# Kernel tuning notes

Hardware: AMD Instinct MI355X
Metric: run time of the kernel (lower is better)

The kernel has to match this reference:

```python
import jax, jax.numpy as jnp
import numpy as np

C = 256
H = 8
D = C // H


def setup_inputs() -> dict:
    key = jax.random.key(0)
    ks = jax.random.split(key, 6)
    scale = 1.0 / np.sqrt(C)
    x = jax.random.normal(ks[0], (8, C, 2048), dtype=jnp.float32)
    Wq = jax.random.normal(ks[1], (C, C), dtype=jnp.float32) * scale
    Wk = jax.random.normal(ks[2], (C, C), dtype=jnp.float32) * scale
    Wv = jax.random.normal(ks[3], (C, C), dtype=jnp.float32) * scale
    Wo = jax.random.normal(ks[4], (C, C), dtype=jnp.float32) * scale
    bo = jax.random.normal(ks[5], (C,), dtype=jnp.float32) * 0.01
    return {"x": x, "Wq": Wq, "Wk": Wk, "Wv": Wv, "Wo": Wo, "bo": bo}


def reference(x, Wq, Wk, Wv, Wo, bo):
    # x: [N, C, L]; Conv1d(k=1) == per-position matmul with weight [out, in]
    q = jnp.einsum('oc,ncl->nol', Wq, x)
    k = jnp.einsum('oc,ncl->nol', Wk, x)
    v = jnp.einsum('oc,ncl->nol', Wv, x)
    N, _, L = x.shape
    # rearrange 'n (h d) l -> n l h d'
    q = q.reshape(N, H, D, L).transpose(0, 3, 1, 2)
    k = k.reshape(N, H, D, L).transpose(0, 3, 1, 2)
    v = v.reshape(N, H, D, L).transpose(0, 3, 1, 2)
    qk = jnp.einsum('nqhd,nkhd->nhqk', q, k)
    # NOTE: original scales by full embedding size (channels), not head_dim
    attn = jax.nn.softmax(qk * (C ** -0.5), axis=3)
    out = jnp.einsum('nhql,nlhd->nqhd', attn, v)
    # rearrange 'n l h d -> n (h d) l'
    out = out.transpose(0, 2, 3, 1).reshape(N, C, L)
    return jnp.einsum('oc,ncl->nol', Wo, out) + bo[None, :, None]
```

## Files before the change

### kernel.cpp

```cpp
#include <hip/hip_runtime.h>


typedef __bf16 bf8 __attribute__((ext_vector_type(8)));
typedef float f4 __attribute__((ext_vector_type(4)));
typedef float f32x4 __attribute__((ext_vector_type(4)));
typedef unsigned short u16;
typedef unsigned int u32;
typedef u16 u16x4 __attribute__((ext_vector_type(4)));
typedef u16 u16x8 __attribute__((ext_vector_type(8)));
typedef u32 u32x4 __attribute__((ext_vector_type(4)));

__device__ __forceinline__ u16 f2bf(float f) {
  __bf16 h = (__bf16)f;
  return __builtin_bit_cast(u16, h);
}
__device__ __forceinline__ float bf2f(u16 b) {
  union { u32 u; float f; } v; v.u = ((u32)b) << 16;
  return v.f;
}
__device__ __forceinline__ u32 pk2bf(float a, float b) {
  return ((u32)f2bf(b) << 16) | (u32)f2bf(a);
}
__device__ __forceinline__ float exp2_fast(float x) {
  return __builtin_amdgcn_exp2f(x);
}

#define MFMA(a, b, c) __builtin_amdgcn_mfma_f32_16x16x32_bf16((a), (b), (c), 0, 0, 0)

__global__ __launch_bounds__(256) void convert_weights(
    const float* __restrict__ Wq, const float* __restrict__ Wk,
    const float* __restrict__ Wv, const float* __restrict__ Wo,
    const float* __restrict__ bo,
    u16* __restrict__ Wqb, u16* __restrict__ Wkb, u16* __restrict__ Wvb,
    u16* __restrict__ Wob, u16* __restrict__ bob) {
  const int tid = threadIdx.x;
  const int seg = blockIdx.x >> 6;
  const int blk = blockIdx.x & 63;
  const float* s; u16* d;
  if (seg == 0)      { s = Wq; d = Wqb; }
  else if (seg == 1) { s = Wk; d = Wkb; }
  else if (seg == 2) { s = Wv; d = Wvb; }
  else               { s = Wo; d = Wob; }
  const int base = blk * 1024 + tid * 4;
  f32x4 v = *(const f32x4*)(s + base);
  u16x4 o;
#pragma unroll
  for (int i = 0; i < 4; ++i) o[i] = f2bf(v[i]);
  *(u16x4*)(d + base) = o;
  if (blockIdx.x == 0 && tid < 64) {
    const int bb = tid * 4;
    f32x4 bv = *(const f32x4*)(bo + bb);
    u16x4 ob;
#pragma unroll
    for (int i = 0; i < 4; ++i) ob[i] = f2bf(bv[i]);
    *(u16x4*)(bob + bb) = ob;
  }
}

__global__ __launch_bounds__(256) void qkv_proj(
    const float* __restrict__ x, const u16* __restrict__ Wq,
    const u16* __restrict__ Wk, const u16* __restrict__ Wv,
    u16* __restrict__ qbuf, u16* __restrict__ kbuf, u16* __restrict__ vbuf) {
  __shared__ __align__(16) u16 xt[2][64 * 40];
  const int n = blockIdx.z;
  const int o0 = blockIdx.y * 64;
  const int l0 = blockIdx.x * 64;
  const int tid = threadIdx.x;
  const int w = tid >> 6, lane = tid & 63, quad = lane >> 4, l16 = lane & 15;
  const int ow = o0 + w * 16;

  f4 acc[3][4];
#pragma unroll
  for (int p = 0; p < 3; ++p)
#pragma unroll
    for (int lt = 0; lt < 4; ++lt) acc[p][lt] = (f4){0.f, 0.f, 0.f, 0.f};

  const int cp = tid >> 4;
  const int lq = (tid & 15) * 4;

  auto stage = [&](int c0, int buf) {
    const float* xp = x + (n * 256 + c0 + 2 * cp) * 2048 + l0 + lq;
    f32x4 r0 = *(const f32x4*)xp;
    f32x4 r1 = *(const f32x4*)(xp + 2048);
#pragma unroll
    for (int i = 0; i < 4; ++i)
      *(u32*)&xt[buf][(lq + i) * 40 + 2 * cp] = pk2bf(r0[i], r1[i]);
  };

  stage(0, 0);
  for (int s = 0; s < 8; ++s) {
    __syncthreads();
    if (s < 7) stage((s + 1) * 32, (s + 1) & 1);
    const int c0 = s * 32;
    bf8 a0 = *(const bf8*)(Wq + (ow + l16) * 256 + c0 + quad * 8);
    bf8 a1 = *(const bf8*)(Wk + (ow + l16) * 256 + c0 + quad * 8);
    bf8 a2 = *(const bf8*)(Wv + (ow + l16) * 256 + c0 + quad * 8);
    const u16* xb = xt[s & 1];
#pragma unroll
    for (int lt = 0; lt < 4; ++lt) {
      bf8 b = *(const bf8*)&xb[(lt * 16 + l16) * 40 + quad * 8];
      acc[0][lt] = MFMA(a0, b, acc[0][lt]);
      acc[1][lt] = MFMA(a1, b, acc[1][lt]);
      acc[2][lt] = MFMA(a2, b, acc[2][lt]);
    }
  }
#pragma unroll
  for (int lt = 0; lt < 4; ++lt) {
    const int l = l0 + lt * 16 + l16;
#pragma unroll
    for (int r = 0; r < 4; ++r) {
      const int o = ow + quad * 4 + r;
      const int qk_idx = ((n * 8 + (o >> 5)) * 2048 + l) * 32 + (o & 31);
      qbuf[qk_idx] = f2bf(acc[0][lt][r]);
      kbuf[qk_idx] = f2bf(acc[1][lt][r]);
      vbuf[(n * 256 + o) * 2048 + l] = f2bf(acc[2][lt][r]);
    }
  }
}

__global__ __launch_bounds__(256) void attn(
    const u16* __restrict__ qbuf, const u16* __restrict__ kbuf,
    const u16* __restrict__ vbuf, u16* __restrict__ abuf) {
  __shared__ __align__(16) u16 Klds[64 * 40];
  __shared__ __align__(16) u32 Vlds[32 * 36];
  __shared__ __align__(16) u32 Pb[4][32 * 36];
  const int head = blockIdx.x;
  const int n = head >> 3, h = head & 7;
  const int tid = threadIdx.x;
  const int w = tid >> 6, lane = tid & 63, quad = lane >> 4, l16 = lane & 15;
  const int q0 = blockIdx.y * 128 + w * 32;

  const u16* kb = kbuf + (size_t)head * 2048 * 32;
  const u16* vb = vbuf + ((size_t)n * 256 + h * 32) * 2048;
  u32* pb32 = Pb[w];
  const u16* pbu = (const u16*)Pb[w];
  const u16* vld16 = (const u16*)Vlds;

  bf8 aq[2];
  aq[0] = *(const bf8*)(qbuf + ((size_t)head * 2048 + q0 + l16) * 32 + quad * 8);
  aq[1] = *(const bf8*)(qbuf + ((size_t)head * 2048 + q0 + 16 + l16) * 32 + quad * 8);

  f4 O[2][2];
  float lsum[2][4];
#pragma unroll
  for (int qt = 0; qt < 2; ++qt) {
    O[qt][0] = (f4){0.f, 0.f, 0.f, 0.f};
    O[qt][1] = (f4){0.f, 0.f, 0.f, 0.f};
#pragma unroll
    for (int r = 0; r < 4; ++r) lsum[qt][r] = 0.f;
  }

  const int krow = tid >> 2, kcol = (tid & 3) * 8;
  const int vd = tid >> 3, vg = (tid & 7) >> 2, vcb = (tid & 3) * 4;

  const float SC = 0.09019327066650391f;

  for (int kc = 0; kc < 2048; kc += 64) {
    __syncthreads();
    *(u16x8*)&Klds[krow * 40 + kcol] = *(const u16x8*)(kb + (kc + krow) * 32 + kcol);
    {
      const u16* vp = vb + vd * 2048 + kc + vg * 32 + vcb;
      u16x4 lo = *(const u16x4*)vp;
      u16x4 hi = *(const u16x4*)(vp + 16);
      u32x4 pk;
#pragma unroll
      for (int i = 0; i < 4; ++i) pk[i] = ((u32)hi[i] << 16) | (u32)lo[i];
      *(u32x4*)&Vlds[vd * 36 + vg * 16 + vcb] = pk;
    }
    __syncthreads();

    bf8 bk[4];
#pragma unroll
    for (int b = 0; b < 4; ++b)
      bk[b] = *(const bf8*)&Klds[(b * 16 + l16) * 40 + quad * 8];

#pragma unroll
    for (int qt = 0; qt < 2; ++qt) {
      f4 z = (f4){0.f, 0.f, 0.f, 0.f};
      f4 s0 = MFMA(aq[qt], bk[0], z);
      f4 s1 = MFMA(aq[qt], bk[1], z);
      f4 s2 = MFMA(aq[qt], bk[2], z);
      f4 s3 = MFMA(aq[qt], bk[3], z);
      const int rowb = (qt * 16 + quad * 4) * 36 + l16;
#pragma unroll
      for (int r = 0; r < 4; ++r) {
        float e00 = exp2_fast(s0[r] * SC);
        float e01 = exp2_fast(s1[r] * SC);
        float e10 = exp2_fast(s2[r] * SC);
        float e11 = exp2_fast(s3[r] * SC);
        lsum[qt][r] += (e00 + e01) + (e10 + e11);
        pb32[rowb + r * 36]      = pk2bf(e00, e01);
        pb32[rowb + r * 36 + 16] = pk2bf(e10, e11);
      }
    }
    asm volatile("s_waitcnt lgkmcnt(0)" ::: "memory");
#pragma unroll
    for (int g = 0; g < 2; ++g) {
      bf8 bv0 = *(const bf8*)&vld16[l16 * 72 + g * 32 + quad * 8];
      bf8 bv1 = *(const bf8*)&vld16[(16 + l16) * 72 + g * 32 + quad * 8];
      bf8 ap0 = *(const bf8*)&pbu[l16 * 72 + g * 32 + quad * 8];
      bf8 ap1 = *(const bf8*)&pbu[(16 + l16) * 72 + g * 32 + quad * 8];
      O[0][0] = MFMA(ap0, bv0, O[0][0]);
      O[0][1] = MFMA(ap0, bv1, O[0][1]);
      O[1][0] = MFMA(ap1, bv0, O[1][0]);
      O[1][1] = MFMA(ap1, bv1, O[1][1]);
    }
  }

#pragma unroll
  for (int qt = 0; qt < 2; ++qt)
#pragma unroll
    for (int r = 0; r < 4; ++r) {
      float s = lsum[qt][r];
      s += __shfl_xor(s, 1);
      s += __shfl_xor(s, 2);
      s += __shfl_xor(s, 4);
      s += __shfl_xor(s, 8);
      const float inv = 1.0f / s;
      const int q = q0 + qt * 16 + quad * 4 + r;
#pragma unroll
      for (int dt = 0; dt < 2; ++dt) {
        const int d = dt * 16 + l16;
        abuf[((size_t)n * 2048 + q) * 256 + h * 32 + d] = f2bf(O[qt][dt][r] * inv);
      }
    }
}

__global__ __launch_bounds__(256) void out_proj(
    const u16* __restrict__ abuf, const u16* __restrict__ Wo,
    const u16* __restrict__ bo, float* __restrict__ out) {
  const int n = blockIdx.z;
  const int o0 = blockIdx.y * 64;
  const int l0 = blockIdx.x * 64;
  const int tid = threadIdx.x;
  const int w = tid >> 6, lane = tid & 63, quad = lane >> 4, l16 = lane & 15;
  const int ow = o0 + w * 16;

  f4 acc[4];
#pragma unroll
  for (int lt = 0; lt < 4; ++lt) acc[lt] = (f4){0.f, 0.f, 0.f, 0.f};

  for (int c0 = 0; c0 < 256; c0 += 32) {
    bf8 a = *(const bf8*)(Wo + (ow + l16) * 256 + c0 + quad * 8);
#pragma unroll
    for (int lt = 0; lt < 4; ++lt) {
      bf8 b = *(const bf8*)(abuf + ((size_t)n * 2048 + l0 + lt * 16 + l16) * 256 + c0 + quad * 8);
      acc[lt] = MFMA(a, b, acc[lt]);
    }
  }
#pragma unroll
  for (int r = 0; r < 4; ++r) {
    const int o = ow + quad * 4 + r;
    const float bias = bf2f(bo[o]);
#pragma unroll
    for (int lt = 0; lt < 4; ++lt) {
      out[((size_t)n * 256 + o) * 2048 + l0 + lt * 16 + l16] = acc[lt][r] + bias;
    }
  }
}

extern "C" void kernel_launch(void* const* d_in, const int* in_sizes, int n_in,
                              void* d_out, int out_size, void* d_ws, size_t ws_size,
                              hipStream_t stream) {
  const float* x  = (const float*)d_in[0];
  const float* Wq = (const float*)d_in[1];
  const float* Wk = (const float*)d_in[2];
  const float* Wv = (const float*)d_in[3];
  const float* Wo = (const float*)d_in[4];
  const float* bo = (const float*)d_in[5];
  float* out = (float*)d_out;

  u16* ws = (u16*)d_ws;
  u16* qbuf = ws;
  u16* kbuf = qbuf + 4194304;
  u16* vbuf = kbuf + 4194304;
  u16* abuf = vbuf + 4194304;
  u16* Wqb  = abuf + 4194304;
  u16* Wkb  = Wqb + 65536;
  u16* Wvb  = Wkb + 65536;
  u16* Wob  = Wvb + 65536;
  u16* bob  = Wob + 65536;

  convert_weights<<<dim3(256), 256, 0, stream>>>(Wq, Wk, Wv, Wo, bo,
                                                 Wqb, Wkb, Wvb, Wob, bob);
  qkv_proj<<<dim3(32, 4, 8), 256, 0, stream>>>(x, Wqb, Wkb, Wvb,
                                               qbuf, kbuf, vbuf);
  attn<<<dim3(64, 16), 256, 0, stream>>>(qbuf, kbuf, vbuf, abuf);
  out_proj<<<dim3(32, 4, 8), 256, 0, stream>>>(abuf, Wob, bob, out);
}
```

Before: 204.6 us.

## Load K/V fragments directly from global into registers with prefetch, dropping LDS staging

The attention kernel no longer stages K and V tiles through shared memory with two block barriers per chunk. Each lane now loads its MFMA fragments straight from global memory and prefetches the next chunk into registers. To make the V loads contiguous, qkv_proj writes V in an interleaved position order. The softmax scale is folded into Q at projection time, and the grid is transposed so query blocks of the same head are adjacent. This removes barriers and LDS traffic, at the cost of redundant global/L2 loads across the four waves and higher register pressure.

After: 225.0 us. 1.1x slower.

```diff
diff --git a/kernel.cpp b/kernel.cpp
--- a/kernel.cpp
+++ b/kernel.cpp
@@ -8,7 +8,6 @@
 typedef unsigned int u32;
 typedef u16 u16x4 __attribute__((ext_vector_type(4)));
 typedef u16 u16x8 __attribute__((ext_vector_type(8)));
-typedef u32 u32x4 __attribute__((ext_vector_type(4)));
 
 __device__ __forceinline__ u16 f2bf(float f) {
   __bf16 h = (__bf16)f;
@@ -68,6 +67,7 @@
   const int tid = threadIdx.x;
   const int w = tid >> 6, lane = tid & 63, quad = lane >> 4, l16 = lane & 15;
   const int ow = o0 + w * 16;
+  const float SC = 0.09019327066650391f;
 
   f4 acc[3][4];
 #pragma unroll
@@ -107,13 +107,14 @@
 #pragma unroll
   for (int lt = 0; lt < 4; ++lt) {
     const int l = l0 + lt * 16 + l16;
+    const int vpos = l0 + (lt >> 1) * 32 + 2 * l16 + (lt & 1);
 #pragma unroll
     for (int r = 0; r < 4; ++r) {
       const int o = ow + quad * 4 + r;
       const int qk_idx = ((n * 8 + (o >> 5)) * 2048 + l) * 32 + (o & 31);
-      qbuf[qk_idx] = f2bf(acc[0][lt][r]);
+      qbuf[qk_idx] = f2bf(acc[0][lt][r] * SC);
       kbuf[qk_idx] = f2bf(acc[1][lt][r]);
-      vbuf[(n * 256 + o) * 2048 + l] = f2bf(acc[2][lt][r]);
+      vbuf[(n * 256 + o) * 2048 + vpos] = f2bf(acc[2][lt][r]);
     }
   }
 }
@@ -121,20 +122,17 @@
 __global__ __launch_bounds__(256) void attn(
     const u16* __restrict__ qbuf, const u16* __restrict__ kbuf,
     const u16* __restrict__ vbuf, u16* __restrict__ abuf) {
-  __shared__ __align__(16) u16 Klds[64 * 40];
-  __shared__ __align__(16) u32 Vlds[32 * 36];
   __shared__ __align__(16) u32 Pb[4][32 * 36];
-  const int head = blockIdx.x;
+  const int qblk = blockIdx.x, head = blockIdx.y;
   const int n = head >> 3, h = head & 7;
   const int tid = threadIdx.x;
   const int w = tid >> 6, lane = tid & 63, quad = lane >> 4, l16 = lane & 15;
-  const int q0 = blockIdx.y * 128 + w * 32;
-
-  const u16* kb = kbuf + (size_t)head * 2048 * 32;
-  const u16* vb = vbuf + ((size_t)n * 256 + h * 32) * 2048;
+  const int q0 = qblk * 128 + w * 32;
+
+  const u16* kb = kbuf + (size_t)head * 2048 * 32 + l16 * 32 + quad * 8;
+  const u16* vb = vbuf + ((size_t)n * 256 + h * 32 + l16) * 2048 + quad * 8;
   u32* pb32 = Pb[w];
   const u16* pbu = (const u16*)Pb[w];
-  const u16* vld16 = (const u16*)Vlds;
 
   bf8 aq[2];
   aq[0] = *(const bf8*)(qbuf + ((size_t)head * 2048 + q0 + l16) * 32 + quad * 8);
@@ -150,29 +148,27 @@
     for (int r = 0; r < 4; ++r) lsum[qt][r] = 0.f;
   }
 
-  const int krow = tid >> 2, kcol = (tid & 3) * 8;
-  const int vd = tid >> 3, vg = (tid & 7) >> 2, vcb = (tid & 3) * 4;
-
-  const float SC = 0.09019327066650391f;
+  bf8 bk[4], bv[4];
+#pragma unroll
+  for (int b = 0; b < 4; ++b) bk[b] = *(const bf8*)(kb + b * 16 * 32);
+#pragma unroll
+  for (int dt = 0; dt < 2; ++dt)
+#pragma unroll
+    for (int g = 0; g < 2; ++g)
+      bv[dt * 2 + g] = *(const bf8*)(vb + dt * 16 * 2048 + g * 32);
 
   for (int kc = 0; kc < 2048; kc += 64) {
-    __syncthreads();
-    *(u16x8*)&Klds[krow * 40 + kcol] = *(const u16x8*)(kb + (kc + krow) * 32 + kcol);
-    {
-      const u16* vp = vb + vd * 2048 + kc + vg * 32 + vcb;
-      u16x4 lo = *(const u16x4*)vp;
-      u16x4 hi = *(const u16x4*)(vp + 16);
-      u32x4 pk;
-#pragma unroll
-      for (int i = 0; i < 4; ++i) pk[i] = ((u32)hi[i] << 16) | (u32)lo[i];
-      *(u32x4*)&Vlds[vd * 36 + vg * 16 + vcb] = pk;
-    }
-    __syncthreads();
-
-    bf8 bk[4];
-#pragma unroll
-    for (int b = 0; b < 4; ++b)
-      bk[b] = *(const bf8*)&Klds[(b * 16 + l16) * 40 + quad * 8];
+    bf8 nk[4], nv[4];
+    const int kn = kc + 64;
+    if (kn < 2048) {
+#pragma unroll
+      for (int b = 0; b < 4; ++b) nk[b] = *(const bf8*)(kb + (kn + b * 16) * 32);
+#pragma unroll
+      for (int dt = 0; dt < 2; ++dt)
+#pragma unroll
+        for (int g = 0; g < 2; ++g)
+          nv[dt * 2 + g] = *(const bf8*)(vb + dt * 16 * 2048 + kn + g * 32);
+    }
 
 #pragma unroll
     for (int qt = 0; qt < 2; ++qt) {
@@ -184,10 +180,10 @@
       const int rowb = (qt * 16 + quad * 4) * 36 + l16;
 #pragma unroll
       for (int r = 0; r < 4; ++r) {
-        float e00 = exp2_fast(s0[r] * SC);
-        float e01 = exp2_fast(s1[r] * SC);
-        float e10 = exp2_fast(s2[r] * SC);
-        float e11 = exp2_fast(s3[r] * SC);
+        float e00 = exp2_fast(s0[r]);
+        float e01 = exp2_fast(s1[r]);
+        float e10 = exp2_fast(s2[r]);
+        float e11 = exp2_fast(s3[r]);
         lsum[qt][r] += (e00 + e01) + (e10 + e11);
         pb32[rowb + r * 36]      = pk2bf(e00, e01);
         pb32[rowb + r * 36 + 16] = pk2bf(e10, e11);
@@ -196,15 +192,15 @@
     asm volatile("s_waitcnt lgkmcnt(0)" ::: "memory");
 #pragma unroll
     for (int g = 0; g < 2; ++g) {
-      bf8 bv0 = *(const bf8*)&vld16[l16 * 72 + g * 32 + quad * 8];
-      bf8 bv1 = *(const bf8*)&vld16[(16 + l16) * 72 + g * 32 + quad * 8];
       bf8 ap0 = *(const bf8*)&pbu[l16 * 72 + g * 32 + quad * 8];
       bf8 ap1 = *(const bf8*)&pbu[(16 + l16) * 72 + g * 32 + quad * 8];
-      O[0][0] = MFMA(ap0, bv0, O[0][0]);
-      O[0][1] = MFMA(ap0, bv1, O[0][1]);
-      O[1][0] = MFMA(ap1, bv0, O[1][0]);
-      O[1][1] = MFMA(ap1, bv1, O[1][1]);
-    }
+      O[0][0] = MFMA(ap0, bv[g], O[0][0]);
+      O[0][1] = MFMA(ap0, bv[2 + g], O[0][1]);
+      O[1][0] = MFMA(ap1, bv[g], O[1][0]);
+      O[1][1] = MFMA(ap1, bv[2 + g], O[1][1]);
+    }
+#pragma unroll
+    for (int i = 0; i < 4; ++i) { bk[i] = nk[i]; bv[i] = nv[i]; }
   }
 
 #pragma unroll
@@ -285,6 +281,6 @@
                                                  Wqb, Wkb, Wvb, Wob, bob);
   qkv_proj<<<dim3(32, 4, 8), 256, 0, stream>>>(x, Wqb, Wkb, Wvb,
                                                qbuf, kbuf, vbuf);
-  attn<<<dim3(64, 16), 256, 0, stream>>>(qbuf, kbuf, vbuf, abuf);
+  attn<<<dim3(16, 64), 256, 0, stream>>>(qbuf, kbuf, vbuf, abuf);
   out_proj<<<dim3(32, 4, 8), 256, 0, stream>>>(abuf, Wob, bob, out);
 }
```
